# Kernel optimization log

Measured on AMD Instinct MI355X. Metric: run time of the kernel, lower is better.

Reference implementation:

```python
import jax, jax.numpy as jnp
import numpy as np

N = 8192      # total QM atoms (concatenated over batch)
L = 6         # num_interactions / trajectory length
F = 256       # hidden_size
FH = F // 2
D_RBF = 32    # distance_embedding_size
E = 131072    # total probe edges
P = 32768     # total probes
CUTOFF = 4.0


def silu(x):
    return x * jax.nn.sigmoid(x)


def setup_inputs() -> dict:
    key = jax.random.key(0)
    ks = jax.random.split(key, 20)
    g = lambda k, shp, s=1.0: jax.random.normal(k, shp, dtype=jnp.float32) * s
    s_stack = g(ks[0], (N, L, F))
    v_stack = g(ks[1], (N, L, 3, F))
    # positions in a 2A box so all probe-atom distances < cutoff=4A
    atom_xyz = jax.random.uniform(ks[2], (N, 3), dtype=jnp.float32) * 2.0
    probe_xyz = jax.random.uniform(ks[3], (P, 3), dtype=jnp.float32) * 2.0
    cell = jnp.eye(3, dtype=jnp.float32) * 2.0
    probe_edges_displacement = jnp.zeros((E, 3), dtype=jnp.float32)
    atom_idx = jax.random.randint(ks[4], (E,), 0, N)
    probe_idx = jax.random.randint(ks[5], (E,), 0, P)
    probe_edges = jnp.stack([atom_idx, probe_idx], axis=1)
    in_dim = D_RBF + 3 * F  # e_pi || q_pi || n_i || S_JK
    return {
        's_stack': s_stack,
        'v_stack': v_stack,
        'atom_xyz': atom_xyz,
        'probe_xyz': probe_xyz,
        'cell': cell,
        'probe_edges_displacement': probe_edges_displacement,
        # JK attention MLP: F -> F/2 -> 1
        'attn_w1': g(ks[6], (F, FH), 1.0 / np.sqrt(F)),
        'attn_b1': jnp.zeros((FH,), jnp.float32),
        'attn_w2': g(ks[7], (FH, 1), 1.0 / np.sqrt(FH)),
        'attn_b2': jnp.zeros((1,), jnp.float32),
        # readout msg MLP: (D_rbf+3F) -> F -> F/2 -> 1
        'msg_w1': g(ks[8], (in_dim, F), 1.0 / np.sqrt(in_dim)),
        'msg_b1': jnp.zeros((F,), jnp.float32),
        'msg_w2': g(ks[9], (F, FH), 1.0 / np.sqrt(F)),
        'msg_b2': jnp.zeros((FH,), jnp.float32),
        'msg_w3': g(ks[10], (FH, 1), 1.0 / np.sqrt(FH)),
        'msg_b3': jnp.zeros((1,), jnp.float32),
        'probe_edges': probe_edges,
    }


def reference(s_stack, v_stack, atom_xyz, probe_xyz, cell, probe_edges_displacement,
              attn_w1, attn_b1, attn_w2, attn_b2,
              msg_w1, msg_b1, msg_w2, msg_b2, msg_w3, msg_b3,
              probe_edges):
    # ---- JKNetAggregation: node-level attention over layer trajectory ----
    h = silu(jnp.einsum('nlf,fh->nlh', s_stack, attn_w1) + attn_b1)   # [N,L,F/2]
    logits = (jnp.einsum('nlh,ho->nlo', h, attn_w2) + attn_b2)[..., 0]  # [N,L]
    a = jax.nn.softmax(logits, axis=1)                                  # [N,L]
    S_JK = jnp.einsum('nl,nlf->nf', a, s_stack)                         # [N,F]
    V_JK = jnp.einsum('nl,nlcf->ncf', a, v_stack)                       # [N,3,F]

    # ---- InfoBottleneckReadout: gather -> per-edge MLP -> scatter ----
    atom_idx = probe_edges[:, 0]
    probe_idx = probe_edges[:, 1]
    shift = probe_edges_displacement @ cell                             # [E,3] PBC shift
    diff = probe_xyz[probe_idx] - (atom_xyz[atom_idx] + shift)          # [E,3]
    dist = jnp.linalg.norm(diff, axis=-1)                               # [E]
    d = dist[:, None]
    n = jnp.arange(1, D_RBF + 1, dtype=jnp.float32)
    e_pi = jnp.sin(d * n * jnp.pi / CUTOFF) / (d + 1e-8)                # [E,D_rbf] sinc RBF
    r_hat = diff / (d + 1e-8)                                           # [E,3]
    V_e = V_JK[atom_idx]                                                # [E,3,F]
    q_pi = jnp.einsum('ecf,ec->ef', V_e, r_hat)                         # [E,F]
    n_i = jnp.linalg.norm(V_JK, axis=1)                                 # [N,F]
    h_pi = jnp.concatenate([e_pi, q_pi, n_i[atom_idx], S_JK[atom_idx]], axis=-1)  # [E,D_rbf+3F]
    m = silu(h_pi @ msg_w1 + msg_b1)
    m = silu(m @ msg_w2 + msg_b2)
    m = (m @ msg_w3 + msg_b3)[:, 0]                                     # [E]
    cw = jnp.where(dist < CUTOFF, 0.5 * (jnp.cos(jnp.pi * dist / CUTOFF) + 1.0), 0.0)
    rho = jax.ops.segment_sum(m * cw, probe_idx, num_segments=P)        # [P]
    return rho
```

## Files before the change

kernel.cpp:

```cpp
#include <hip/hip_runtime.h>
#include <math.h>
#include <stdint.h>


#define L_DIM 6
#define F_DIM 256
#define FH_DIM 128
#define DRBF 32
#define CUTOFF_F 4.0f
#define PI_F 3.14159265358979323846f

using bf16x8 = __attribute__((ext_vector_type(8))) short;
using f32x4v = __attribute__((ext_vector_type(4))) float;

__device__ __forceinline__ float silu_f(float x){ return x / (1.f + __expf(-x)); }

__device__ __forceinline__ unsigned short f2bf(float f){
    uint32_t u = __float_as_uint(f);
    uint32_t r = (u + 0x7fffu + ((u >> 16) & 1u)) >> 16;
    return (unsigned short)r;
}

__global__ __launch_bounds__(256) void kPrep(
    const float* __restrict__ msg_w1, const float* __restrict__ msg_w2,
    const float* __restrict__ attn_w1,
    unsigned short* __restrict__ w1bt, unsigned short* __restrict__ w1cdt,
    unsigned short* __restrict__ w2t, unsigned short* __restrict__ wA1t)
{
    int idx = blockIdx.x * 256 + threadIdx.x;
    if (idx < 65536){
        int k = idx >> 8, j = idx & 255;
        w1bt[(size_t)j * 256 + k] = f2bf(msg_w1[(size_t)(DRBF + k) * F_DIM + j]);
    } else if (idx < 196608){
        int i2 = idx - 65536;
        int k = i2 >> 8, j = i2 & 255;
        w1cdt[(size_t)j * 512 + k] = f2bf(msg_w1[(size_t)(DRBF + 256 + k) * F_DIM + j]);
    } else if (idx < 229376){
        int i3 = idx - 196608;
        int k = i3 >> 7, h = i3 & 127;
        w2t[(size_t)h * 256 + k] = f2bf(msg_w2[(size_t)k * FH_DIM + h]);
    } else {
        int i4 = idx - 229376;
        int j = i4 >> 8, k = i4 & 255;
        wA1t[(size_t)j * 256 + k] = f2bf(attn_w1[(size_t)k * FH_DIM + j]);
    }
}

__global__ __launch_bounds__(256) void kL(
    const float* __restrict__ s2d, const unsigned short* __restrict__ wA1t,
    const float* __restrict__ attn_b1, const float* __restrict__ attn_w2,
    float* __restrict__ LG)
{
    __shared__ float part[4][64];

    const int t  = threadIdx.x;
    const int l  = t & 63;
    const int w  = t >> 6;
    const int lm = l & 15, lq = l >> 4;

    bf16x8 bfr[2][8];
    #pragma unroll
    for (int nt2 = 0; nt2 < 2; nt2++){
        const int col = w*32 + nt2*16 + lm;
        #pragma unroll
        for (int kb = 0; kb < 8; kb++)
            bfr[nt2][kb] = *(const bf16x8*)(wA1t + (size_t)col * 256 + kb*32 + lq*8);
    }
    const float b1a = attn_b1[w*32 + lm];
    const float b1b = attn_b1[w*32 + 16 + lm];
    const float w2a = attn_w2[w*32 + lm];
    const float w2b = attn_w2[w*32 + 16 + lm];

    const int r00 = blockIdx.x * 64;

    #pragma unroll
    for (int mt = 0; mt < 4; mt++){
        const int r0 = r00 + mt * 16;
        bf16x8 af[8];
        #pragma unroll
        for (int kb = 0; kb < 8; kb++){
            const float* ap = s2d + (size_t)(r0 + lm) * 256 + kb*32 + lq*8;
            float4 fa = *(const float4*)ap;
            float4 fb = *(const float4*)(ap + 4);
            bf16x8 v;
            v[0] = (short)f2bf(fa.x); v[1] = (short)f2bf(fa.y);
            v[2] = (short)f2bf(fa.z); v[3] = (short)f2bf(fa.w);
            v[4] = (short)f2bf(fb.x); v[5] = (short)f2bf(fb.y);
            v[6] = (short)f2bf(fb.z); v[7] = (short)f2bf(fb.w);
            af[kb] = v;
        }
        f32x4v a0 = {0.f,0.f,0.f,0.f}, a1 = {0.f,0.f,0.f,0.f};
        #pragma unroll
        for (int kb = 0; kb < 8; kb++){
            a0 = __builtin_amdgcn_mfma_f32_16x16x32_bf16(af[kb], bfr[0][kb], a0, 0, 0, 0);
            a1 = __builtin_amdgcn_mfma_f32_16x16x32_bf16(af[kb], bfr[1][kb], a1, 0, 0, 0);
        }
        #pragma unroll
        for (int r = 0; r < 4; r++){
            float p = silu_f(a0[r] + b1a) * w2a + silu_f(a1[r] + b1b) * w2b;
            #pragma unroll
            for (int m = 8; m >= 1; m >>= 1) p += __shfl_xor(p, m, 64);
            if (lm == 0) part[w][mt*16 + lq*4 + r] = p;
        }
    }
    __syncthreads();
    if (t < 64)
        LG[r00 + t] = part[0][t] + part[1][t] + part[2][t] + part[3][t];
}

__global__ __launch_bounds__(256) void kW(
    const float* __restrict__ s_stack, const float* __restrict__ v_stack,
    const float* __restrict__ LG,
    unsigned short* __restrict__ VJKb, unsigned short* __restrict__ NISb, int N)
{
    const int t    = threadIdx.x;
    const int w    = t >> 6;
    const int lane = t & 63;
    const int n    = min(blockIdx.x * 4 + w, N - 1);

    float aw[L_DIM];
    #pragma unroll
    for (int l = 0; l < L_DIM; l++) aw[l] = LG[(size_t)n * L_DIM + l];
    float mx = aw[0];
    #pragma unroll
    for (int l = 1; l < L_DIM; l++) mx = fmaxf(mx, aw[l]);
    float sum = 0.f;
    #pragma unroll
    for (int l = 0; l < L_DIM; l++){ aw[l] = __expf(aw[l] - mx); sum += aw[l]; }
    const float inv = 1.f / sum;
    #pragma unroll
    for (int l = 0; l < L_DIM; l++) aw[l] *= inv;

    const float* sp = s_stack + (size_t)n * (L_DIM * F_DIM) + lane * 4;
    const float* vp = v_stack + (size_t)n * (L_DIM * 3 * F_DIM) + lane * 4;
    float4 v0 = {0.f,0.f,0.f,0.f}, v1 = {0.f,0.f,0.f,0.f}, v2 = {0.f,0.f,0.f,0.f};
    float4 sj = {0.f,0.f,0.f,0.f};
    #pragma unroll
    for (int l = 0; l < L_DIM; l++){
        const float a = aw[l];
        float4 ss = *(const float4*)(sp + (size_t)l * F_DIM);
        float4 x0 = *(const float4*)(vp + (size_t)(l*3+0) * F_DIM);
        float4 x1 = *(const float4*)(vp + (size_t)(l*3+1) * F_DIM);
        float4 x2 = *(const float4*)(vp + (size_t)(l*3+2) * F_DIM);
        v0.x = fmaf(a, x0.x, v0.x); v0.y = fmaf(a, x0.y, v0.y);
        v0.z = fmaf(a, x0.z, v0.z); v0.w = fmaf(a, x0.w, v0.w);
        v1.x = fmaf(a, x1.x, v1.x); v1.y = fmaf(a, x1.y, v1.y);
        v1.z = fmaf(a, x1.z, v1.z); v1.w = fmaf(a, x1.w, v1.w);
        v2.x = fmaf(a, x2.x, v2.x); v2.y = fmaf(a, x2.y, v2.y);
        v2.z = fmaf(a, x2.z, v2.z); v2.w = fmaf(a, x2.w, v2.w);
        sj.x = fmaf(a, ss.x, sj.x); sj.y = fmaf(a, ss.y, sj.y);
        sj.z = fmaf(a, ss.z, sj.z); sj.w = fmaf(a, ss.w, sj.w);
    }
    float4 ni;
    ni.x = sqrtf(v0.x*v0.x + v1.x*v1.x + v2.x*v2.x);
    ni.y = sqrtf(v0.y*v0.y + v1.y*v1.y + v2.y*v2.y);
    ni.z = sqrtf(v0.z*v0.z + v1.z*v1.z + v2.z*v2.z);
    ni.w = sqrtf(v0.w*v0.w + v1.w*v1.w + v2.w*v2.w);

    ushort4 o;
    o = (ushort4){f2bf(v0.x), f2bf(v0.y), f2bf(v0.z), f2bf(v0.w)};
    *(ushort4*)&VJKb[((size_t)n*3 + 0) * F_DIM + lane*4] = o;
    o = (ushort4){f2bf(v1.x), f2bf(v1.y), f2bf(v1.z), f2bf(v1.w)};
    *(ushort4*)&VJKb[((size_t)n*3 + 1) * F_DIM + lane*4] = o;
    o = (ushort4){f2bf(v2.x), f2bf(v2.y), f2bf(v2.z), f2bf(v2.w)};
    *(ushort4*)&VJKb[((size_t)n*3 + 2) * F_DIM + lane*4] = o;
    o = (ushort4){f2bf(ni.x), f2bf(ni.y), f2bf(ni.z), f2bf(ni.w)};
    *(ushort4*)&NISb[(size_t)n * 512 + lane*4] = o;
    o = (ushort4){f2bf(sj.x), f2bf(sj.y), f2bf(sj.z), f2bf(sj.w)};
    *(ushort4*)&NISb[(size_t)n * 512 + 256 + lane*4] = o;
}

__global__ __launch_bounds__(256) void kA2u(
    const unsigned short* __restrict__ VJKb, const unsigned short* __restrict__ w1bt,
    float* __restrict__ UT4, int M)
{
    const int t  = threadIdx.x;
    const int l  = t & 63;
    const int w  = t >> 6;
    const int lm = l & 15, lq = l >> 4;

    bf16x8 bfr[4][8];
    #pragma unroll
    for (int ct = 0; ct < 4; ct++)
        #pragma unroll
        for (int kb = 0; kb < 8; kb++)
            bfr[ct][kb] = *(const bf16x8*)(w1bt + (size_t)(w*64 + ct*16 + lm) * 256 + kb*32 + lq*8);

    const int r00 = blockIdx.x * 128;
    #pragma unroll 1
    for (int mt = 0; mt < 8; mt++){
        const int r0 = r00 + mt * 16;
        bf16x8 af[8];
        #pragma unroll
        for (int kb = 0; kb < 8; kb++)
            af[kb] = *(const bf16x8*)(VJKb + (size_t)(r0 + lm) * 256 + kb*32 + lq*8);
        f32x4v acc[4];
        #pragma unroll
        for (int ct = 0; ct < 4; ct++) acc[ct] = (f32x4v){0.f,0.f,0.f,0.f};
        #pragma unroll
        for (int kb = 0; kb < 8; kb++)
            #pragma unroll
            for (int ct = 0; ct < 4; ct++)
                acc[ct] = __builtin_amdgcn_mfma_f32_16x16x32_bf16(af[kb], bfr[ct][kb], acc[ct], 0, 0, 0);
        #pragma unroll
        for (int ct = 0; ct < 4; ct++){
            const int col = w*64 + ct*16 + lm;
            #pragma unroll
            for (int r = 0; r < 4; r++){
                const int row = r0 + lq*4 + r;
                const int n = row / 3, c = row - n*3;
                UT4[(((size_t)n << 8) + col) * 4 + c] = acc[ct][r];
            }
        }
    }
}

__global__ __launch_bounds__(256) void kA2t(
    const unsigned short* __restrict__ NISb, const unsigned short* __restrict__ w1cdt,
    const float* __restrict__ msg_b1,
    float* __restrict__ UT4, int M)
{
    const int t  = threadIdx.x;
    const int l  = t & 63;
    const int w  = t >> 6;
    const int lm = l & 15, lq = l >> 4;

    const int ch = blockIdx.x & 1;
    const int bm = blockIdx.x >> 1;

    bf16x8 bfr[2][16];
    #pragma unroll
    for (int ct = 0; ct < 2; ct++)
        #pragma unroll
        for (int kb = 0; kb < 16; kb++)
            bfr[ct][kb] = *(const bf16x8*)(w1cdt + (size_t)(ch*128 + w*32 + ct*16 + lm) * 512 + kb*32 + lq*8);

    const int r00 = bm * 128;
    #pragma unroll 1
    for (int mt = 0; mt < 8; mt++){
        const int r0 = r00 + mt * 16;
        bf16x8 af[16];
        #pragma unroll
        for (int kb = 0; kb < 16; kb++)
            af[kb] = *(const bf16x8*)(NISb + (size_t)(r0 + lm) * 512 + kb*32 + lq*8);
        f32x4v acc[2];
        #pragma unroll
        for (int ct = 0; ct < 2; ct++) acc[ct] = (f32x4v){0.f,0.f,0.f,0.f};
        #pragma unroll
        for (int kb = 0; kb < 16; kb++)
            #pragma unroll
            for (int ct = 0; ct < 2; ct++)
                acc[ct] = __builtin_amdgcn_mfma_f32_16x16x32_bf16(af[kb], bfr[ct][kb], acc[ct], 0, 0, 0);
        #pragma unroll
        for (int ct = 0; ct < 2; ct++){
            const int col = ch*128 + w*32 + ct*16 + lm;
            const float bias = msg_b1[col];
            #pragma unroll
            for (int r = 0; r < 4; r++){
                const int n = r0 + lq*4 + r;
                UT4[(((size_t)n << 8) + col) * 4 + 3] = acc[ct][r] + bias;
            }
        }
    }
}

__global__ __launch_bounds__(256) void kHist(const int* __restrict__ pe, int* __restrict__ cnt, int E){
    int e = blockIdx.x * 256 + threadIdx.x;
    if (e < E) atomicAdd(&cnt[pe[(size_t)e*2]], 1);
}

__global__ __launch_bounds__(1024) void kScan(const int* __restrict__ cnt, int* __restrict__ off, int N){
    __shared__ int sums[1024];
    const int t = threadIdx.x;
    const int base = t * 8;
    int c[8]; int s = 0;
    #pragma unroll
    for (int j = 0; j < 8; j++){
        int v = (base + j < N) ? cnt[base + j] : 0;
        c[j] = s; s += v;
    }
    sums[t] = s;
    __syncthreads();
    for (int d = 1; d < 1024; d <<= 1){
        int v = (t >= d) ? sums[t - d] : 0;
        __syncthreads();
        sums[t] += v;
        __syncthreads();
    }
    int excl = (t == 0) ? 0 : sums[t - 1];
    #pragma unroll
    for (int j = 0; j < 8; j++)
        if (base + j < N) off[base + j] = excl + c[j];
    if (t == 1023) off[N] = sums[1023];
}

__global__ __launch_bounds__(256) void kScatter(const int* __restrict__ pe,
    const int* __restrict__ off, int* __restrict__ pos, int* __restrict__ perm, int E){
    int e = blockIdx.x * 256 + threadIdx.x;
    if (e < E){
        int i = pe[(size_t)e*2];
        int slot = atomicAdd(&pos[i], 1);
        perm[off[i] + slot] = e;
    }
}

__global__ __launch_bounds__(256) void kB1(
    const int* __restrict__ pe, const float* __restrict__ disp,
    const float* __restrict__ cell,
    const float* __restrict__ atom_xyz, const float* __restrict__ probe_xyz,
    const float* __restrict__ UT4,
    const float* __restrict__ msg_w1,
    const unsigned short* __restrict__ w2t, const float* __restrict__ msg_b2,
    const float* __restrict__ msg_w3, const float* __restrict__ msg_b3,
    const int* __restrict__ perm,
    float* __restrict__ rho, int E)
{
    __shared__ unsigned short x_lds[32 * 256];
    __shared__ unsigned short epi_b[32 * 40];
    __shared__ int   ai_l[32];
    __shared__ int   pp_l[32];
    __shared__ float4 rc4_l[32];
    __shared__ float part[4][32];

    char* xbase = (char*)x_lds;

    const int t  = threadIdx.x;
    const int l  = t & 63;
    const int w  = t >> 6;
    const int lq = l >> 4;
    const int lm = l & 15;

    const float c0 = cell[0], c1 = cell[1], c2 = cell[2];
    const float c3 = cell[3], c4 = cell[4], c5 = cell[5];
    const float c6 = cell[6], c7 = cell[7], c8 = cell[8];

    bf16x8 w1afr[4];
    #pragma unroll
    for (int nt = 0; nt < 4; nt++){
        const int col = w*64 + nt*16 + lm;
        bf16x8 v;
        #pragma unroll
        for (int j = 0; j < 8; j++)
            v[j] = (short)f2bf(msg_w1[(size_t)(lq*8 + j) * F_DIM + col]);
        w1afr[nt] = v;
    }

    bf16x8 bfr[2][8];
    #pragma unroll
    for (int nt2 = 0; nt2 < 2; nt2++){
        const int h = w*32 + nt2*16 + lm;
        #pragma unroll
        for (int kb = 0; kb < 8; kb++)
            bfr[nt2][kb] = *(const bf16x8*)(w2t + (size_t)h * F_DIM + kb*32 + lq*8);
    }
    const float b2v0 = msg_b2[w*32 + lm];
    const float b2v1 = msg_b2[w*32 + 16 + lm];
    const float w3v0 = msg_w3[w*32 + lm];
    const float w3v1 = msg_w3[w*32 + 16 + lm];
    const float b3   = msg_b3[0];

    const int e0 = blockIdx.x * 128;

    int ee_r[4], ia_r[4], ip_r[4];
    #pragma unroll
    for (int bb = 0; bb < 4; bb++){
        int s = min(e0 + bb*32 + (t >> 3), E - 1);
        ee_r[bb] = perm[s];
    }
    #pragma unroll
    for (int bb = 0; bb < 4; bb++){
        ia_r[bb] = pe[(size_t)ee_r[bb]*2];
        ip_r[bb] = pe[(size_t)ee_r[bb]*2 + 1];
    }

    #pragma unroll 1
    for (int bb = 0; bb < 4; bb++){
        const int e0b = e0 + bb * 32;

        {
            const int slot = t >> 3, q = t & 7;
            const int ee = ee_r[bb];
            const int ia = ia_r[bb];
            const int ip = ip_r[bb];
            const float d0 = disp[(size_t)ee*3], d1 = disp[(size_t)ee*3+1], d2 = disp[(size_t)ee*3+2];
            const float sx = d0*c0 + d1*c3 + d2*c6;
            const float sy = d0*c1 + d1*c4 + d2*c7;
            const float sz = d0*c2 + d1*c5 + d2*c8;
            const float dx = probe_xyz[(size_t)ip*3+0] - (atom_xyz[(size_t)ia*3+0] + sx);
            const float dy = probe_xyz[(size_t)ip*3+1] - (atom_xyz[(size_t)ia*3+1] + sy);
            const float dz = probe_xyz[(size_t)ip*3+2] - (atom_xyz[(size_t)ia*3+2] + sz);
            const float dist = sqrtf(dx*dx + dy*dy + dz*dz);
            const float inv  = 1.f / (dist + 1e-8f);
            const float base = dist * (PI_F / CUTOFF_F);
            ushort4 eb;
            eb.x = f2bf(__sinf(base * (float)(q*4 + 1)) * inv);
            eb.y = f2bf(__sinf(base * (float)(q*4 + 2)) * inv);
            eb.z = f2bf(__sinf(base * (float)(q*4 + 3)) * inv);
            eb.w = f2bf(__sinf(base * (float)(q*4 + 4)) * inv);
            *(ushort4*)&epi_b[slot*40 + q*4] = eb;
            if (q == 0){
                ai_l[slot] = ia;
                pp_l[slot] = ip;
                float cw = (dist < CUTOFF_F) ? 0.5f * (__cosf(base) + 1.f) : 0.f;
                rc4_l[slot] = (float4){dx*inv, dy*inv, dz*inv, cw};
            }
        }
        __syncthreads();

        f32x4v pacc[2][4];
        #pragma unroll
        for (int mt = 0; mt < 2; mt++)
            #pragma unroll
            for (int nt = 0; nt < 4; nt++) pacc[mt][nt] = (f32x4v){0.f,0.f,0.f,0.f};
        #pragma unroll
        for (int mt = 0; mt < 2; mt++){
            const bf16x8 af = *(const bf16x8*)&epi_b[(mt*16 + lm)*40 + lq*8];
            #pragma unroll
            for (int nt = 0; nt < 4; nt++)
                pacc[mt][nt] = __builtin_amdgcn_mfma_f32_16x16x32_bf16(af, w1afr[nt], pacc[mt][nt], 0, 0, 0);
        }

        #pragma unroll
        for (int mt = 0; mt < 2; mt++){
            #pragma unroll
            for (int r = 0; r < 4; r++){
                const int e = mt*16 + lq*4 + r;
                const int i = ai_l[e];
                const float4 rc = rc4_l[e];
                const float* up = UT4 + ((size_t)i << 10);
                #pragma unroll
                for (int nt = 0; nt < 4; nt++){
                    const int col = w*64 + nt*16 + lm;
                    const float4 ut = *(const float4*)(up + (size_t)col * 4);
                    float z = pacc[mt][nt][r] + ut.w;
                    z = fmaf(rc.x, ut.x, fmaf(rc.y, ut.y, fmaf(rc.z, ut.z, z)));
                    const int wofs = e*512 + ((col*2) ^ ((e & 7) << 4));
                    *(unsigned short*)(xbase + wofs) = f2bf(silu_f(z));
                }
            }
        }
        __syncthreads();

        f32x4v acc00 = {0.f,0.f,0.f,0.f}, acc01 = {0.f,0.f,0.f,0.f};
        f32x4v acc10 = {0.f,0.f,0.f,0.f}, acc11 = {0.f,0.f,0.f,0.f};
        const int eA0 = lm;
        const int eA1 = 16 + lm;
        #pragma unroll
        for (int kb = 0; kb < 8; kb++){
            const int ko = kb*64 + lq*16;
            bf16x8 af0 = *(const bf16x8*)(xbase + eA0*512 + (ko ^ ((eA0 & 7) << 4)));
            bf16x8 af1 = *(const bf16x8*)(xbase + eA1*512 + (ko ^ ((eA1 & 7) << 4)));
            acc00 = __builtin_amdgcn_mfma_f32_16x16x32_bf16(af0, bfr[0][kb], acc00, 0, 0, 0);
            acc01 = __builtin_amdgcn_mfma_f32_16x16x32_bf16(af0, bfr[1][kb], acc01, 0, 0, 0);
            acc10 = __builtin_amdgcn_mfma_f32_16x16x32_bf16(af1, bfr[0][kb], acc10, 0, 0, 0);
            acc11 = __builtin_amdgcn_mfma_f32_16x16x32_bf16(af1, bfr[1][kb], acc11, 0, 0, 0);
        }

        float pr0[4], pr1[4];
        #pragma unroll
        for (int r = 0; r < 4; r++){
            pr0[r] = silu_f(acc00[r] + b2v0) * w3v0 + silu_f(acc01[r] + b2v1) * w3v1;
            pr1[r] = silu_f(acc10[r] + b2v0) * w3v0 + silu_f(acc11[r] + b2v1) * w3v1;
        }
        #pragma unroll
        for (int r = 0; r < 4; r++){
            #pragma unroll
            for (int m = 8; m >= 1; m >>= 1){
                pr0[r] += __shfl_xor(pr0[r], m, 64);
                pr1[r] += __shfl_xor(pr1[r], m, 64);
            }
        }
        if (lm == 0){
            #pragma unroll
            for (int r = 0; r < 4; r++){
                part[w][lq*4 + r]      = pr0[r];
                part[w][16 + lq*4 + r] = pr1[r];
            }
        }
        __syncthreads();

        if (t < 32 && (e0b + t) < E){
            float tot = part[0][t] + part[1][t] + part[2][t] + part[3][t] + b3;
            atomicAdd(&rho[pp_l[t]], tot * rc4_l[t].w);
        }
        __syncthreads();
    }
}

extern "C" void kernel_launch(void* const* d_in, const int* in_sizes, int n_in,
                              void* d_out, int out_size, void* d_ws, size_t ws_size,
                              hipStream_t stream)
{
    const float* s_stack   = (const float*)d_in[0];
    const float* v_stack   = (const float*)d_in[1];
    const float* atom_xyz  = (const float*)d_in[2];
    const float* probe_xyz = (const float*)d_in[3];
    const float* cell      = (const float*)d_in[4];
    const float* disp      = (const float*)d_in[5];
    const float* attn_w1   = (const float*)d_in[6];
    const float* attn_b1   = (const float*)d_in[7];
    const float* attn_w2   = (const float*)d_in[8];
    const float* msg_w1    = (const float*)d_in[10];
    const float* msg_b1    = (const float*)d_in[11];
    const float* msg_w2    = (const float*)d_in[12];
    const float* msg_b2    = (const float*)d_in[13];
    const float* msg_w3    = (const float*)d_in[14];
    const float* msg_b3    = (const float*)d_in[15];
    const int*   pe        = (const int*)d_in[16];

    const int N = in_sizes[0] / (L_DIM * F_DIM);
    const int E = in_sizes[16] / 2;
    const int P = out_size;
    const size_t NF = (size_t)N * F_DIM;

    float* ws = (float*)d_ws;
    unsigned short* VJKb = (unsigned short*)ws;
    unsigned short* NISb = VJKb + 3*NF;
    float* UT4 = ws + (5*NF)/2;
    unsigned short* w1bt  = (unsigned short*)(ws + (13*NF)/2);
    unsigned short* w1cdt = w1bt + 65536;
    unsigned short* w2t   = w1cdt + 131072;
    unsigned short* wA1t  = w2t + 32768;
    float* LG  = (float*)(wA1t + 32768);
    int* cnt  = (int*)(LG + (size_t)N * L_DIM);
    int* pos  = cnt + N;
    int* offs = pos + N;
    int* perm = offs + N + 1;

    hipMemsetAsync(d_out, 0, (size_t)P * sizeof(float), stream);
    hipMemsetAsync(cnt, 0, 2 * (size_t)N * sizeof(int), stream);

    kPrep<<<1024, 256, 0, stream>>>(msg_w1, msg_w2, attn_w1, w1bt, w1cdt, w2t, wA1t);

    kL<<<(N * L_DIM) / 64, 256, 0, stream>>>(s_stack, wA1t, attn_b1, attn_w2, LG);
    kW<<<(N + 3) / 4, 256, 0, stream>>>(s_stack, v_stack, LG, VJKb, NISb, N);

    kA2u<<<(3 * N) / 128, 256, 0, stream>>>(VJKb, w1bt, UT4, 3 * N);
    kA2t<<<(N / 128) * 2, 256, 0, stream>>>(NISb, w1cdt, msg_b1, UT4, N);

    const int gE = (E + 255) / 256;
    kHist<<<gE, 256, 0, stream>>>(pe, cnt, E);
    kScan<<<1, 1024, 0, stream>>>(cnt, offs, N);
    kScatter<<<gE, 256, 0, stream>>>(pe, offs, pos, perm, E);

    kB1<<<(E + 127) / 128, 256, 0, stream>>>(pe, disp, cell, atom_xyz, probe_xyz,
                                             UT4, msg_w1,
                                             w2t, msg_b2, msg_w3, msg_b3,
                                             perm, (float*)d_out, E);
}
```

Before: 208.1 us.

## Fuse attention logits with JK weighting; enlarge edge tiles and prefetch gathers in kB1

Merges the attention-logit kernel and the softmax-weighted JK aggregation into one kernel, so logits stay in shared memory instead of going through a global LG buffer, and one launch is removed. Each block handles 16 atoms with 96 MFMA rows, then applies the softmax and the weighted sum over layers. The edge kernel kB1 now processes 64-edge sub-tiles, two per block instead of four of 32. It prefetches the next sub-tile's perm, index and coordinate gathers into registers while the current one is computed, and drops a trailing barrier. The costs are more shared memory and registers per block, which may lower occupancy, and fewer blocks in the fused kernel.

```diff
diff --git a/kernel.cpp b/kernel.cpp
--- a/kernel.cpp
+++ b/kernel.cpp
@@ -46,12 +46,14 @@
     }
 }
 
-__global__ __launch_bounds__(256) void kL(
-    const float* __restrict__ s2d, const unsigned short* __restrict__ wA1t,
+__global__ __launch_bounds__(256) void kAW(
+    const float* __restrict__ s_stack, const float* __restrict__ v_stack,
+    const unsigned short* __restrict__ wA1t,
     const float* __restrict__ attn_b1, const float* __restrict__ attn_w2,
-    float* __restrict__ LG)
+    unsigned short* __restrict__ VJKb, unsigned short* __restrict__ NISb, int N)
 {
-    __shared__ float part[4][64];
+    __shared__ float part[4][96];
+    __shared__ float aw_l[16][8];
 
     const int t  = threadIdx.x;
     const int l  = t & 63;
@@ -71,15 +73,18 @@
     const float w2a = attn_w2[w*32 + lm];
     const float w2b = attn_w2[w*32 + 16 + lm];
 
-    const int r00 = blockIdx.x * 64;
-
-    #pragma unroll
-    for (int mt = 0; mt < 4; mt++){
-        const int r0 = r00 + mt * 16;
+    const int n0 = blockIdx.x * 16;
+    const size_t rbase = (size_t)n0 * L_DIM;
+    const size_t rmax  = (size_t)N * L_DIM - 1;
+
+    #pragma unroll
+    for (int mt = 0; mt < 6; mt++){
+        const size_t r0 = rbase + mt * 16;
         bf16x8 af[8];
         #pragma unroll
         for (int kb = 0; kb < 8; kb++){
-            const float* ap = s2d + (size_t)(r0 + lm) * 256 + kb*32 + lq*8;
+            size_t row = r0 + lm; if (row > rmax) row = rmax;
+            const float* ap = s_stack + row * 256 + kb*32 + lq*8;
             float4 fa = *(const float4*)ap;
             float4 fb = *(const float4*)(ap + 4);
             bf16x8 v;
@@ -104,70 +109,66 @@
         }
     }
     __syncthreads();
-    if (t < 64)
-        LG[r00 + t] = part[0][t] + part[1][t] + part[2][t] + part[3][t];
-}
-
-__global__ __launch_bounds__(256) void kW(
-    const float* __restrict__ s_stack, const float* __restrict__ v_stack,
-    const float* __restrict__ LG,
-    unsigned short* __restrict__ VJKb, unsigned short* __restrict__ NISb, int N)
-{
-    const int t    = threadIdx.x;
-    const int w    = t >> 6;
-    const int lane = t & 63;
-    const int n    = min(blockIdx.x * 4 + w, N - 1);
-
-    float aw[L_DIM];
-    #pragma unroll
-    for (int l = 0; l < L_DIM; l++) aw[l] = LG[(size_t)n * L_DIM + l];
-    float mx = aw[0];
-    #pragma unroll
-    for (int l = 1; l < L_DIM; l++) mx = fmaxf(mx, aw[l]);
-    float sum = 0.f;
-    #pragma unroll
-    for (int l = 0; l < L_DIM; l++){ aw[l] = __expf(aw[l] - mx); sum += aw[l]; }
-    const float inv = 1.f / sum;
-    #pragma unroll
-    for (int l = 0; l < L_DIM; l++) aw[l] *= inv;
-
-    const float* sp = s_stack + (size_t)n * (L_DIM * F_DIM) + lane * 4;
-    const float* vp = v_stack + (size_t)n * (L_DIM * 3 * F_DIM) + lane * 4;
-    float4 v0 = {0.f,0.f,0.f,0.f}, v1 = {0.f,0.f,0.f,0.f}, v2 = {0.f,0.f,0.f,0.f};
-    float4 sj = {0.f,0.f,0.f,0.f};
-    #pragma unroll
-    for (int l = 0; l < L_DIM; l++){
-        const float a = aw[l];
-        float4 ss = *(const float4*)(sp + (size_t)l * F_DIM);
-        float4 x0 = *(const float4*)(vp + (size_t)(l*3+0) * F_DIM);
-        float4 x1 = *(const float4*)(vp + (size_t)(l*3+1) * F_DIM);
-        float4 x2 = *(const float4*)(vp + (size_t)(l*3+2) * F_DIM);
-        v0.x = fmaf(a, x0.x, v0.x); v0.y = fmaf(a, x0.y, v0.y);
-        v0.z = fmaf(a, x0.z, v0.z); v0.w = fmaf(a, x0.w, v0.w);
-        v1.x = fmaf(a, x1.x, v1.x); v1.y = fmaf(a, x1.y, v1.y);
-        v1.z = fmaf(a, x1.z, v1.z); v1.w = fmaf(a, x1.w, v1.w);
-        v2.x = fmaf(a, x2.x, v2.x); v2.y = fmaf(a, x2.y, v2.y);
-        v2.z = fmaf(a, x2.z, v2.z); v2.w = fmaf(a, x2.w, v2.w);
-        sj.x = fmaf(a, ss.x, sj.x); sj.y = fmaf(a, ss.y, sj.y);
-        sj.z = fmaf(a, ss.z, sj.z); sj.w = fmaf(a, ss.w, sj.w);
-    }
-    float4 ni;
-    ni.x = sqrtf(v0.x*v0.x + v1.x*v1.x + v2.x*v2.x);
-    ni.y = sqrtf(v0.y*v0.y + v1.y*v1.y + v2.y*v2.y);
-    ni.z = sqrtf(v0.z*v0.z + v1.z*v1.z + v2.z*v2.z);
-    ni.w = sqrtf(v0.w*v0.w + v1.w*v1.w + v2.w*v2.w);
-
-    ushort4 o;
-    o = (ushort4){f2bf(v0.x), f2bf(v0.y), f2bf(v0.z), f2bf(v0.w)};
-    *(ushort4*)&VJKb[((size_t)n*3 + 0) * F_DIM + lane*4] = o;
-    o = (ushort4){f2bf(v1.x), f2bf(v1.y), f2bf(v1.z), f2bf(v1.w)};
-    *(ushort4*)&VJKb[((size_t)n*3 + 1) * F_DIM + lane*4] = o;
-    o = (ushort4){f2bf(v2.x), f2bf(v2.y), f2bf(v2.z), f2bf(v2.w)};
-    *(ushort4*)&VJKb[((size_t)n*3 + 2) * F_DIM + lane*4] = o;
-    o = (ushort4){f2bf(ni.x), f2bf(ni.y), f2bf(ni.z), f2bf(ni.w)};
-    *(ushort4*)&NISb[(size_t)n * 512 + lane*4] = o;
-    o = (ushort4){f2bf(sj.x), f2bf(sj.y), f2bf(sj.z), f2bf(sj.w)};
-    *(ushort4*)&NISb[(size_t)n * 512 + 256 + lane*4] = o;
+    if (t < 96) part[0][t] = part[0][t] + part[1][t] + part[2][t] + part[3][t];
+    __syncthreads();
+    if (t < 16){
+        float e[L_DIM]; float mx = -1e30f;
+        #pragma unroll
+        for (int l6 = 0; l6 < L_DIM; l6++) mx = fmaxf(mx, part[0][t*L_DIM + l6]);
+        float s = 0.f;
+        #pragma unroll
+        for (int l6 = 0; l6 < L_DIM; l6++){ e[l6] = __expf(part[0][t*L_DIM + l6] - mx); s += e[l6]; }
+        float inv = 1.f / s;
+        #pragma unroll
+        for (int l6 = 0; l6 < L_DIM; l6++) aw_l[t][l6] = e[l6] * inv;
+    }
+    __syncthreads();
+
+    #pragma unroll 1
+    for (int aa = 0; aa < 4; aa++){
+        const int n = min(n0 + w*4 + aa, N - 1);
+        float aw[L_DIM];
+        #pragma unroll
+        for (int l6 = 0; l6 < L_DIM; l6++) aw[l6] = aw_l[w*4 + aa][l6];
+
+        const float* sp = s_stack + (size_t)n * (L_DIM * F_DIM) + l * 4;
+        const float* vp = v_stack + (size_t)n * (L_DIM * 3 * F_DIM) + l * 4;
+        float4 v0 = {0.f,0.f,0.f,0.f}, v1 = {0.f,0.f,0.f,0.f}, v2 = {0.f,0.f,0.f,0.f};
+        float4 sj = {0.f,0.f,0.f,0.f};
+        #pragma unroll
+        for (int l6 = 0; l6 < L_DIM; l6++){
+            const float a = aw[l6];
+            float4 ss = *(const float4*)(sp + (size_t)l6 * F_DIM);
+            float4 x0 = *(const float4*)(vp + (size_t)(l6*3+0) * F_DIM);
+            float4 x1 = *(const float4*)(vp + (size_t)(l6*3+1) * F_DIM);
+            float4 x2 = *(const float4*)(vp + (size_t)(l6*3+2) * F_DIM);
+            v0.x = fmaf(a, x0.x, v0.x); v0.y = fmaf(a, x0.y, v0.y);
+            v0.z = fmaf(a, x0.z, v0.z); v0.w = fmaf(a, x0.w, v0.w);
+            v1.x = fmaf(a, x1.x, v1.x); v1.y = fmaf(a, x1.y, v1.y);
+            v1.z = fmaf(a, x1.z, v1.z); v1.w = fmaf(a, x1.w, v1.w);
+            v2.x = fmaf(a, x2.x, v2.x); v2.y = fmaf(a, x2.y, v2.y);
+            v2.z = fmaf(a, x2.z, v2.z); v2.w = fmaf(a, x2.w, v2.w);
+            sj.x = fmaf(a, ss.x, sj.x); sj.y = fmaf(a, ss.y, sj.y);
+            sj.z = fmaf(a, ss.z, sj.z); sj.w = fmaf(a, ss.w, sj.w);
+        }
+        float4 ni;
+        ni.x = sqrtf(v0.x*v0.x + v1.x*v1.x + v2.x*v2.x);
+        ni.y = sqrtf(v0.y*v0.y + v1.y*v1.y + v2.y*v2.y);
+        ni.z = sqrtf(v0.z*v0.z + v1.z*v1.z + v2.z*v2.z);
+        ni.w = sqrtf(v0.w*v0.w + v1.w*v1.w + v2.w*v2.w);
+
+        ushort4 o;
+        o = (ushort4){f2bf(v0.x), f2bf(v0.y), f2bf(v0.z), f2bf(v0.w)};
+        *(ushort4*)&VJKb[((size_t)n*3 + 0) * F_DIM + l*4] = o;
+        o = (ushort4){f2bf(v1.x), f2bf(v1.y), f2bf(v1.z), f2bf(v1.w)};
+        *(ushort4*)&VJKb[((size_t)n*3 + 1) * F_DIM + l*4] = o;
+        o = (ushort4){f2bf(v2.x), f2bf(v2.y), f2bf(v2.z), f2bf(v2.w)};
+        *(ushort4*)&VJKb[((size_t)n*3 + 2) * F_DIM + l*4] = o;
+        o = (ushort4){f2bf(ni.x), f2bf(ni.y), f2bf(ni.z), f2bf(ni.w)};
+        *(ushort4*)&NISb[(size_t)n * 512 + l*4] = o;
+        o = (ushort4){f2bf(sj.x), f2bf(sj.y), f2bf(sj.z), f2bf(sj.w)};
+        *(ushort4*)&NISb[(size_t)n * 512 + 256 + l*4] = o;
+    }
 }
 
 __global__ __launch_bounds__(256) void kA2u(
@@ -315,12 +316,12 @@
     const int* __restrict__ perm,
     float* __restrict__ rho, int E)
 {
-    __shared__ unsigned short x_lds[32 * 256];
-    __shared__ unsigned short epi_b[32 * 40];
-    __shared__ int   ai_l[32];
-    __shared__ int   pp_l[32];
-    __shared__ float4 rc4_l[32];
-    __shared__ float part[4][32];
+    __shared__ unsigned short x_lds[64 * 256];
+    __shared__ unsigned short epi_b[2][64 * 40];
+    __shared__ int   ai_l[2][64];
+    __shared__ int   pp_l[2][64];
+    __shared__ float4 rc4_l[2][64];
+    __shared__ float part[4][64];
 
     char* xbase = (char*)x_lds;
 
@@ -329,6 +330,7 @@
     const int w  = t >> 6;
     const int lq = l >> 4;
     const int lm = l & 15;
+    const int slot = t >> 2, q = t & 3;
 
     const float c0 = cell[0], c1 = cell[1], c2 = cell[2];
     const float c3 = cell[3], c4 = cell[4], c5 = cell[5];
@@ -361,129 +363,141 @@
 
     const int e0 = blockIdx.x * 128;
 
-    int ee_r[4], ia_r[4], ip_r[4];
-    #pragma unroll
-    for (int bb = 0; bb < 4; bb++){
-        int s = min(e0 + bb*32 + (t >> 3), E - 1);
-        ee_r[bb] = perm[s];
-    }
-    #pragma unroll
-    for (int bb = 0; bb < 4; bb++){
-        ia_r[bb] = pe[(size_t)ee_r[bb]*2];
-        ip_r[bb] = pe[(size_t)ee_r[bb]*2 + 1];
-    }
-
-    #pragma unroll 1
-    for (int bb = 0; bb < 4; bb++){
-        const int e0b = e0 + bb * 32;
+    int ee_r[2], ia_r[2], ip_r[2];
+    float gd[2][3], gp[2][3], ga[2][3];
+
+    {
+        int s = min(e0 + slot, E - 1);
+        ee_r[0] = perm[s];
+        ia_r[0] = pe[(size_t)ee_r[0]*2];
+        ip_r[0] = pe[(size_t)ee_r[0]*2 + 1];
+        gd[0][0] = disp[(size_t)ee_r[0]*3];   gd[0][1] = disp[(size_t)ee_r[0]*3+1]; gd[0][2] = disp[(size_t)ee_r[0]*3+2];
+        gp[0][0] = probe_xyz[(size_t)ip_r[0]*3]; gp[0][1] = probe_xyz[(size_t)ip_r[0]*3+1]; gp[0][2] = probe_xyz[(size_t)ip_r[0]*3+2];
+        ga[0][0] = atom_xyz[(size_t)ia_r[0]*3];  ga[0][1] = atom_xyz[(size_t)ia_r[0]*3+1];  ga[0][2] = atom_xyz[(size_t)ia_r[0]*3+2];
+    }
+
+    #pragma unroll
+    for (int bb = 0; bb < 2; bb++){
+        const int e0b = e0 + bb * 64;
 
         {
-            const int slot = t >> 3, q = t & 7;
-            const int ee = ee_r[bb];
-            const int ia = ia_r[bb];
-            const int ip = ip_r[bb];
-            const float d0 = disp[(size_t)ee*3], d1 = disp[(size_t)ee*3+1], d2 = disp[(size_t)ee*3+2];
-            const float sx = d0*c0 + d1*c3 + d2*c6;
-            const float sy = d0*c1 + d1*c4 + d2*c7;
-            const float sz = d0*c2 + d1*c5 + d2*c8;
-            const float dx = probe_xyz[(size_t)ip*3+0] - (atom_xyz[(size_t)ia*3+0] + sx);
-            const float dy = probe_xyz[(size_t)ip*3+1] - (atom_xyz[(size_t)ia*3+1] + sy);
-            const float dz = probe_xyz[(size_t)ip*3+2] - (atom_xyz[(size_t)ia*3+2] + sz);
+            const float sx = gd[bb][0]*c0 + gd[bb][1]*c3 + gd[bb][2]*c6;
+            const float sy = gd[bb][0]*c1 + gd[bb][1]*c4 + gd[bb][2]*c7;
+            const float sz = gd[bb][0]*c2 + gd[bb][1]*c5 + gd[bb][2]*c8;
+            const float dx = gp[bb][0] - (ga[bb][0] + sx);
+            const float dy = gp[bb][1] - (ga[bb][1] + sy);
+            const float dz = gp[bb][2] - (ga[bb][2] + sz);
             const float dist = sqrtf(dx*dx + dy*dy + dz*dz);
             const float inv  = 1.f / (dist + 1e-8f);
             const float base = dist * (PI_F / CUTOFF_F);
-            ushort4 eb;
-            eb.x = f2bf(__sinf(base * (float)(q*4 + 1)) * inv);
-            eb.y = f2bf(__sinf(base * (float)(q*4 + 2)) * inv);
-            eb.z = f2bf(__sinf(base * (float)(q*4 + 3)) * inv);
-            eb.w = f2bf(__sinf(base * (float)(q*4 + 4)) * inv);
-            *(ushort4*)&epi_b[slot*40 + q*4] = eb;
+            ushort4 ea, eb;
+            ea.x = f2bf(__sinf(base * (float)(q*8 + 1)) * inv);
+            ea.y = f2bf(__sinf(base * (float)(q*8 + 2)) * inv);
+            ea.z = f2bf(__sinf(base * (float)(q*8 + 3)) * inv);
+            ea.w = f2bf(__sinf(base * (float)(q*8 + 4)) * inv);
+            eb.x = f2bf(__sinf(base * (float)(q*8 + 5)) * inv);
+            eb.y = f2bf(__sinf(base * (float)(q*8 + 6)) * inv);
+            eb.z = f2bf(__sinf(base * (float)(q*8 + 7)) * inv);
+            eb.w = f2bf(__sinf(base * (float)(q*8 + 8)) * inv);
+            *(ushort4*)&epi_b[bb][slot*40 + q*8]     = ea;
+            *(ushort4*)&epi_b[bb][slot*40 + q*8 + 4] = eb;
             if (q == 0){
-                ai_l[slot] = ia;
-                pp_l[slot] = ip;
+                ai_l[bb][slot] = ia_r[bb];
+                pp_l[bb][slot] = ip_r[bb];
                 float cw = (dist < CUTOFF_F) ? 0.5f * (__cosf(base) + 1.f) : 0.f;
-                rc4_l[slot] = (float4){dx*inv, dy*inv, dz*inv, cw};
-            }
+                rc4_l[bb][slot] = (float4){dx*inv, dy*inv, dz*inv, cw};
+            }
+        }
+
+        if (bb == 0){
+            int s = min(e0 + 64 + slot, E - 1);
+            ee_r[1] = perm[s];
+            ia_r[1] = pe[(size_t)ee_r[1]*2];
+            ip_r[1] = pe[(size_t)ee_r[1]*2 + 1];
+            gd[1][0] = disp[(size_t)ee_r[1]*3];   gd[1][1] = disp[(size_t)ee_r[1]*3+1]; gd[1][2] = disp[(size_t)ee_r[1]*3+2];
+            gp[1][0] = probe_xyz[(size_t)ip_r[1]*3]; gp[1][1] = probe_xyz[(size_t)ip_r[1]*3+1]; gp[1][2] = probe_xyz[(size_t)ip_r[1]*3+2];
+            ga[1][0] = atom_xyz[(size_t)ia_r[1]*3];  ga[1][1] = atom_xyz[(size_t)ia_r[1]*3+1];  ga[1][2] = atom_xyz[(size_t)ia_r[1]*3+2];
         }
         __syncthreads();
 
-        f32x4v pacc[2][4];
-        #pragma unroll
-        for (int mt = 0; mt < 2; mt++)
-            #pragma unroll
-            for (int nt = 0; nt < 4; nt++) pacc[mt][nt] = (f32x4v){0.f,0.f,0.f,0.f};
-        #pragma unroll
-        for (int mt = 0; mt < 2; mt++){
-            const bf16x8 af = *(const bf16x8*)&epi_b[(mt*16 + lm)*40 + lq*8];
-            #pragma unroll
-            for (int nt = 0; nt < 4; nt++)
-                pacc[mt][nt] = __builtin_amdgcn_mfma_f32_16x16x32_bf16(af, w1afr[nt], pacc[mt][nt], 0, 0, 0);
-        }
-
-        #pragma unroll
-        for (int mt = 0; mt < 2; mt++){
-            #pragma unroll
-            for (int r = 0; r < 4; r++){
-                const int e = mt*16 + lq*4 + r;
-                const int i = ai_l[e];
-                const float4 rc = rc4_l[e];
-                const float* up = UT4 + ((size_t)i << 10);
+        #pragma unroll
+        for (int hh = 0; hh < 2; hh++){
+            f32x4v pacc[2][4];
+            #pragma unroll
+            for (int mt = 0; mt < 2; mt++)
                 #pragma unroll
-                for (int nt = 0; nt < 4; nt++){
-                    const int col = w*64 + nt*16 + lm;
-                    const float4 ut = *(const float4*)(up + (size_t)col * 4);
-                    float z = pacc[mt][nt][r] + ut.w;
-                    z = fmaf(rc.x, ut.x, fmaf(rc.y, ut.y, fmaf(rc.z, ut.z, z)));
-                    const int wofs = e*512 + ((col*2) ^ ((e & 7) << 4));
-                    *(unsigned short*)(xbase + wofs) = f2bf(silu_f(z));
+                for (int nt = 0; nt < 4; nt++) pacc[mt][nt] = (f32x4v){0.f,0.f,0.f,0.f};
+            #pragma unroll
+            for (int mt = 0; mt < 2; mt++){
+                const bf16x8 af = *(const bf16x8*)&epi_b[bb][(hh*32 + mt*16 + lm)*40 + lq*8];
+                #pragma unroll
+                for (int nt = 0; nt < 4; nt++)
+                    pacc[mt][nt] = __builtin_amdgcn_mfma_f32_16x16x32_bf16(af, w1afr[nt], pacc[mt][nt], 0, 0, 0);
+            }
+            #pragma unroll
+            for (int mt = 0; mt < 2; mt++){
+                #pragma unroll
+                for (int r = 0; r < 4; r++){
+                    const int e = hh*32 + mt*16 + lq*4 + r;
+                    const int i = ai_l[bb][e];
+                    const float4 rc = rc4_l[bb][e];
+                    const float* up = UT4 + ((size_t)i << 10);
+                    #pragma unroll
+                    for (int nt = 0; nt < 4; nt++){
+                        const int col = w*64 + nt*16 + lm;
+                        const float4 ut = *(const float4*)(up + (size_t)col * 4);
+                        float z = pacc[mt][nt][r] + ut.w;
+                        z = fmaf(rc.x, ut.x, fmaf(rc.y, ut.y, fmaf(rc.z, ut.z, z)));
+                        const int wofs = e*512 + ((col*2) ^ ((e & 7) << 4));
+                        *(unsigned short*)(xbase + wofs) = f2bf(silu_f(z));
+                    }
                 }
             }
         }
         __syncthreads();
 
-        f32x4v acc00 = {0.f,0.f,0.f,0.f}, acc01 = {0.f,0.f,0.f,0.f};
-        f32x4v acc10 = {0.f,0.f,0.f,0.f}, acc11 = {0.f,0.f,0.f,0.f};
-        const int eA0 = lm;
-        const int eA1 = 16 + lm;
+        f32x4v acc[4][2];
+        #pragma unroll
+        for (int m = 0; m < 4; m++){
+            acc[m][0] = (f32x4v){0.f,0.f,0.f,0.f};
+            acc[m][1] = (f32x4v){0.f,0.f,0.f,0.f};
+        }
         #pragma unroll
         for (int kb = 0; kb < 8; kb++){
             const int ko = kb*64 + lq*16;
-            bf16x8 af0 = *(const bf16x8*)(xbase + eA0*512 + (ko ^ ((eA0 & 7) << 4)));
-            bf16x8 af1 = *(const bf16x8*)(xbase + eA1*512 + (ko ^ ((eA1 & 7) << 4)));
-            acc00 = __builtin_amdgcn_mfma_f32_16x16x32_bf16(af0, bfr[0][kb], acc00, 0, 0, 0);
-            acc01 = __builtin_amdgcn_mfma_f32_16x16x32_bf16(af0, bfr[1][kb], acc01, 0, 0, 0);
-            acc10 = __builtin_amdgcn_mfma_f32_16x16x32_bf16(af1, bfr[0][kb], acc10, 0, 0, 0);
-            acc11 = __builtin_amdgcn_mfma_f32_16x16x32_bf16(af1, bfr[1][kb], acc11, 0, 0, 0);
-        }
-
-        float pr0[4], pr1[4];
-        #pragma unroll
-        for (int r = 0; r < 4; r++){
-            pr0[r] = silu_f(acc00[r] + b2v0) * w3v0 + silu_f(acc01[r] + b2v1) * w3v1;
-            pr1[r] = silu_f(acc10[r] + b2v0) * w3v0 + silu_f(acc11[r] + b2v1) * w3v1;
-        }
-        #pragma unroll
-        for (int r = 0; r < 4; r++){
-            #pragma unroll
-            for (int m = 8; m >= 1; m >>= 1){
-                pr0[r] += __shfl_xor(pr0[r], m, 64);
-                pr1[r] += __shfl_xor(pr1[r], m, 64);
-            }
-        }
-        if (lm == 0){
+            #pragma unroll
+            for (int m = 0; m < 4; m++){
+                const int eA = m*16 + lm;
+                bf16x8 af = *(const bf16x8*)(xbase + eA*512 + (ko ^ ((eA & 7) << 4)));
+                acc[m][0] = __builtin_amdgcn_mfma_f32_16x16x32_bf16(af, bfr[0][kb], acc[m][0], 0, 0, 0);
+                acc[m][1] = __builtin_amdgcn_mfma_f32_16x16x32_bf16(af, bfr[1][kb], acc[m][1], 0, 0, 0);
+            }
+        }
+
+        #pragma unroll
+        for (int m = 0; m < 4; m++){
+            float pr[4];
+            #pragma unroll
+            for (int r = 0; r < 4; r++)
+                pr[r] = silu_f(acc[m][0][r] + b2v0) * w3v0 + silu_f(acc[m][1][r] + b2v1) * w3v1;
             #pragma unroll
             for (int r = 0; r < 4; r++){
-                part[w][lq*4 + r]      = pr0[r];
-                part[w][16 + lq*4 + r] = pr1[r];
+                #pragma unroll
+                for (int mm = 8; mm >= 1; mm >>= 1)
+                    pr[r] += __shfl_xor(pr[r], mm, 64);
+            }
+            if (lm == 0){
+                #pragma unroll
+                for (int r = 0; r < 4; r++)
+                    part[w][m*16 + lq*4 + r] = pr[r];
             }
         }
         __syncthreads();
 
-        if (t < 32 && (e0b + t) < E){
+        if (t < 64 && (e0b + t) < E){
             float tot = part[0][t] + part[1][t] + part[2][t] + part[3][t] + b3;
-            atomicAdd(&rho[pp_l[t]], tot * rc4_l[t].w);
-        }
-        __syncthreads();
+            atomicAdd(&rho[pp_l[bb][t]], tot * rc4_l[bb][t].w);
+        }
     }
 }
 
@@ -521,8 +535,7 @@
     unsigned short* w1cdt = w1bt + 65536;
     unsigned short* w2t   = w1cdt + 131072;
     unsigned short* wA1t  = w2t + 32768;
-    float* LG  = (float*)(wA1t + 32768);
-    int* cnt  = (int*)(LG + (size_t)N * L_DIM);
+    int* cnt  = (int*)(wA1t + 32768);
     int* pos  = cnt + N;
     int* offs = pos + N;
     int* perm = offs + N + 1;
@@ -532,8 +545,8 @@
 
     kPrep<<<1024, 256, 0, stream>>>(msg_w1, msg_w2, attn_w1, w1bt, w1cdt, w2t, wA1t);
 
-    kL<<<(N * L_DIM) / 64, 256, 0, stream>>>(s_stack, wA1t, attn_b1, attn_w2, LG);
-    kW<<<(N + 3) / 4, 256, 0, stream>>>(s_stack, v_stack, LG, VJKb, NISb, N);
+    kAW<<<(N + 15) / 16, 256, 0, stream>>>(s_stack, v_stack, wA1t, attn_b1, attn_w2,
+                                           VJKb, NISb, N);
 
     kA2u<<<(3 * N) / 128, 256, 0, stream>>>(VJKb, w1bt, UT4, 3 * N);
     kA2t<<<(N / 128) * 2, 256, 0, stream>>>(NISb, w1cdt, msg_b1, UT4, N);
```

Result: no change. 204.5 us (-1.7%).
